# Optimization experiments

Hardware: AMD Instinct MI355X
Metric: run time of the kernel (lower is better)

## Reference

```python
import jax, jax.numpy as jnp
import numpy as np

EMBED_DIM = 1024
SCALE = 1.0 / float(np.sqrt(EMBED_DIM))


def setup_inputs() -> dict:
    key = jax.random.key(0)
    ks = jax.random.split(key, 7)
    B, S, D = 4, 2048, EMBED_DIM
    init = 1.0 / np.sqrt(D)
    x = jax.random.normal(ks[0], (B, S, D), dtype=jnp.float32)
    Wq = jax.random.uniform(ks[1], (D, D), jnp.float32, -init, init)
    bq = jax.random.uniform(ks[2], (D,), jnp.float32, -init, init)
    Wk = jax.random.uniform(ks[3], (D, D), jnp.float32, -init, init)
    bk = jax.random.uniform(ks[4], (D,), jnp.float32, -init, init)
    Wv = jax.random.uniform(ks[5], (D, D), jnp.float32, -init, init)
    bv = jax.random.uniform(ks[6], (D,), jnp.float32, -init, init)
    return {"x": x, "Wq": Wq, "bq": bq, "Wk": Wk, "bk": bk, "Wv": Wv, "bv": bv}


def reference(x, Wq, bq, Wk, bk, Wv, bv):
    # Linear projections (torch Linear: x @ W.T + b; here W stored as [in, out])
    q = x @ Wq + bq  # [B, S, D]
    k = x @ Wk + bk
    v = x @ Wv + bv
    # Manual scaled dot-product attention (single head)
    scores = jnp.einsum("bsd,btd->bst", q, k) * SCALE  # [B, S, S]
    attn = jax.nn.softmax(scores, axis=-1)
    # Dropout is identity at inference (eval mode); p=0.1 at train time.
    return jnp.einsum("bst,btd->bsd", attn, v)
```

## Files before the change

### kernel.cpp

```cpp
#include <hip/hip_runtime.h>

#define MODE_QKV 0
#define MODE_S   1
#define MODE_PV  2

typedef __attribute__((ext_vector_type(8))) short short8;
typedef __attribute__((ext_vector_type(4))) float floatx4;

typedef const unsigned __attribute__((address_space(1)))* gp_t;
typedef unsigned __attribute__((address_space(3)))* lp_t;

__device__ __forceinline__ void async16(const void* g, void* l) {
  __builtin_amdgcn_global_load_lds((gp_t)g, (lp_t)l, 16, 0, 0);
}

__device__ __forceinline__ unsigned short f2bf(float f) {
  union { float f; unsigned u; } x; x.f = f;
  unsigned r = x.u + 0x7fffu + ((x.u >> 16) & 1u);
  return (unsigned short)(r >> 16);
}
__device__ __forceinline__ float bf2f(unsigned short h) {
  union { unsigned u; float f; } x; x.u = ((unsigned)h) << 16;
  return x.f;
}


__device__ __forceinline__ void stage_half(const unsigned short* gp, long rowbase,
                                           int ldk, int kb, char* region,
                                           int wave, int lane) {
  const int rs = lane >> 3;
  const int kc = ((lane & 7) ^ rs) << 3;
  #pragma unroll
  for (int h = 0; h < 2; h++) {
    const int rr = (h * 8 + wave) * 8 + rs;
    async16(gp + (rowbase + rr) * (long)ldk + kb + kc,
            region + (h * 8 + wave) * 1024);
  }
}

__device__ __forceinline__ short8 frag(const char* region, int hr, int ks, int quad) {
  return *(const short8*)(region + hr * 128 + ((((ks << 2) | quad) ^ (hr & 7)) << 4));
}

#define MFMA_QUAD(MH, NH)                                                    \
  do {                                                                       \
    _Pragma("unroll")                                                        \
    for (int mi_ = 0; mi_ < 4; mi_++) {                                      \
      _Pragma("unroll")                                                      \
      for (int jj_ = 0; jj_ < 2; jj_++) {                                    \
        _Pragma("unroll")                                                    \
        for (int ks_ = 0; ks_ < 2; ks_++) {                                  \
          acc[MH][mi_][NH][jj_] = __builtin_amdgcn_mfma_f32_16x16x32_bf16(   \
              a[mi_][ks_], b[NH][jj_][ks_], acc[MH][mi_][NH][jj_], 0, 0, 0); \
        }                                                                    \
      }                                                                      \
    }                                                                        \
  } while (0)

template<int MODE>
__global__ __launch_bounds__(512, 1)
void gemm256(const unsigned short* __restrict__ A,
             const unsigned short* __restrict__ Bmat,
             const float* __restrict__ b0, const float* __restrict__ b1,
             const float* __restrict__ b2,
             unsigned short* __restrict__ O0, unsigned short* __restrict__ O1,
             unsigned short* __restrict__ O2, float* __restrict__ lsum,
             int M, int N, int K, long aZ, long bZ, long cZ, float scale)
{
  __shared__ __attribute__((aligned(128))) char lds[131072];

  const int tid = threadIdx.x;
  const int wave = tid >> 6, lane = tid & 63;
  const int wm = wave >> 2, wn = wave & 3;
  const int quad = lane >> 4, l16 = lane & 15;

  const int gx = gridDim.x, gy = gridDim.y;
  int z, bm, bn;
  {
    int f = (blockIdx.z * gy + blockIdx.y) * gx + blockIdx.x;
    int T = gx * gy * (int)gridDim.z;
    int nsq = T >> 7;
    int xcd = f & 7, i = f >> 3;
    int sq = xcd * nsq + (i >> 4);
    int w = i & 15;
    int spz = (gx >> 2) * (gy >> 2);
    z = sq / spz;
    int sqr = sq - z * spz;
    int sqm = sqr / (gx >> 2), sqn = sqr - sqm * (gx >> 2);
    bm = (sqm * 4 + (w >> 2)) * 256;
    bn = (sqn * 4 + (w & 3)) * 256;
  }

  const unsigned short* Ap = (MODE == MODE_QKV) ? A : (A + (long)z * aZ);
  const unsigned short* Bp = Bmat + (long)z * bZ;

  const int NT = K >> 6;

  stage_half(Ap, bm,       K, 0,  lds +     0, wave, lane);
  stage_half(Bp, bn,       K, 0,  lds + 32768, wave, lane);
  stage_half(Bp, bn + 128, K, 0,  lds + 49152, wave, lane);
  stage_half(Ap, bm + 128, K, 0,  lds + 16384, wave, lane);
  stage_half(Ap, bm,       K, 64, lds + 65536 +     0, wave, lane);
  stage_half(Bp, bn,       K, 64, lds + 65536 + 32768, wave, lane);
  stage_half(Bp, bn + 128, K, 64, lds + 65536 + 49152, wave, lane);
  asm volatile("s_waitcnt vmcnt(6)" ::: "memory");
  __builtin_amdgcn_s_barrier();

  floatx4 acc[2][4][2][2];
  #pragma unroll
  for (int p = 0; p < 2; p++)
    #pragma unroll
    for (int q2 = 0; q2 < 4; q2++)
      #pragma unroll
      for (int r = 0; r < 2; r++)
        #pragma unroll
        for (int s = 0; s < 2; s++)
          acc[p][q2][r][s] = (floatx4){0.f, 0.f, 0.f, 0.f};

  short8 a[4][2];
  short8 b[2][2][2];

  for (int j = 0; j < NT; j++) {
    char* bufc = lds + ((j & 1) << 16);
    char* bufn = lds + (((j + 1) & 1) << 16);
    const bool lp = (j + 2 >= NT);
    const int kn  = (j + 1) << 6;
    const int kn2 = (j + 2) << 6;

    #pragma unroll
    for (int mi = 0; mi < 4; mi++)
      #pragma unroll
      for (int ks = 0; ks < 2; ks++)
        a[mi][ks] = frag(bufc, wm * 64 + mi * 16 + l16, ks, quad);
    #pragma unroll
    for (int jj = 0; jj < 2; jj++)
      #pragma unroll
      for (int ks = 0; ks < 2; ks++)
        b[0][jj][ks] = frag(bufc + 32768, wn * 32 + jj * 16 + l16, ks, quad);
    if (j + 1 < NT)
      stage_half(Ap, bm + 128, K, kn, bufn + 16384, wave, lane);
    __builtin_amdgcn_s_barrier();
    asm volatile("s_waitcnt lgkmcnt(0)" ::: "memory");
    __builtin_amdgcn_sched_barrier(0);
    __builtin_amdgcn_s_setprio(1);
    MFMA_QUAD(0, 0);
    __builtin_amdgcn_s_setprio(0);
    __builtin_amdgcn_s_barrier();

    #pragma unroll
    for (int jj = 0; jj < 2; jj++)
      #pragma unroll
      for (int ks = 0; ks < 2; ks++)
        b[1][jj][ks] = frag(bufc + 49152, wn * 32 + jj * 16 + l16, ks, quad);
    if (!lp)
      stage_half(Ap, bm, K, kn2, bufc, wave, lane);
    __builtin_amdgcn_s_barrier();
    asm volatile("s_waitcnt lgkmcnt(0)" ::: "memory");
    __builtin_amdgcn_sched_barrier(0);
    __builtin_amdgcn_s_setprio(1);
    MFMA_QUAD(0, 1);
    __builtin_amdgcn_s_setprio(0);
    __builtin_amdgcn_s_barrier();

    #pragma unroll
    for (int mi = 0; mi < 4; mi++)
      #pragma unroll
      for (int ks = 0; ks < 2; ks++)
        a[mi][ks] = frag(bufc + 16384, wm * 64 + mi * 16 + l16, ks, quad);
    if (!lp)
      stage_half(Bp, bn, K, kn2, bufc + 32768, wave, lane);
    __builtin_amdgcn_s_barrier();
    asm volatile("s_waitcnt lgkmcnt(0)" ::: "memory");
    __builtin_amdgcn_sched_barrier(0);
    __builtin_amdgcn_s_setprio(1);
    MFMA_QUAD(1, 0);
    __builtin_amdgcn_s_setprio(0);
    __builtin_amdgcn_s_barrier();

    if (!lp) {
      stage_half(Bp, bn + 128, K, kn2, bufc + 49152, wave, lane);
      asm volatile("s_waitcnt vmcnt(6)" ::: "memory");
    } else {
      asm volatile("s_waitcnt vmcnt(0)" ::: "memory");
    }
    __builtin_amdgcn_s_barrier();
    __builtin_amdgcn_s_setprio(1);
    MFMA_QUAD(1, 1);
    __builtin_amdgcn_s_setprio(0);
    __builtin_amdgcn_s_barrier();
  }

  const bool vtrans = (MODE == MODE_QKV) && (z == 2);
  float bi[2][2];
  if (MODE == MODE_QKV) {
    const float* bias = (z == 0) ? b0 : ((z == 1) ? b1 : b2);
    #pragma unroll
    for (int nh = 0; nh < 2; nh++)
      #pragma unroll
      for (int jj = 0; jj < 2; jj++)
        bi[nh][jj] = bias[bn + nh * 128 + wn * 32 + jj * 16 + l16];
  }

  unsigned short* epi = (unsigned short*)lds;
  #pragma unroll
  for (int mh = 0; mh < 2; mh++) {
    #pragma unroll
    for (int mi = 0; mi < 4; mi++) {
      const int r0 = wm * 64 + mi * 16 + quad * 4;
      #pragma unroll
      for (int nh = 0; nh < 2; nh++)
        #pragma unroll
        for (int jj = 0; jj < 2; jj++) {
          const int col = nh * 128 + wn * 32 + jj * 16 + l16;
          if (MODE == MODE_S) {
            #pragma unroll
            for (int r = 0; r < 4; r++)
              epi[(r0 + r) * 264 + col] = f2bf(__expf(acc[mh][mi][nh][jj][r] * scale));
          } else if (!vtrans) {
            #pragma unroll
            for (int r = 0; r < 4; r++)
              epi[(r0 + r) * 264 + col] = f2bf(acc[mh][mi][nh][jj][r] + bi[nh][jj]);
          } else {
            #pragma unroll
            for (int r = 0; r < 4; r += 2) {
              unsigned lo = f2bf(acc[mh][mi][nh][jj][r] + bi[nh][jj]);
              unsigned hi = f2bf(acc[mh][mi][nh][jj][r + 1] + bi[nh][jj]);
              *(unsigned*)&epi[col * 136 + r0 + r] = lo | (hi << 16);
            }
          }
        }
    }
    __syncthreads();

    if (!vtrans) {
      #pragma unroll
      for (int it = 0; it < 8; it++) {
        int flat = it * 4096 + tid * 8;
        int rr = flat >> 8, cc = flat & 255;
        short8 vline = *(const short8*)&epi[rr * 264 + cc];
        long grow = bm + mh * 128 + rr;
        if (MODE == MODE_S) {
          union { short8 v; unsigned short u[8]; } t; t.v = vline;
          float s8 = 0.f;
          #pragma unroll
          for (int jq = 0; jq < 8; jq++) s8 += bf2f(t.u[jq]);
          s8 += __shfl_xor(s8, 1);
          s8 += __shfl_xor(s8, 2);
          s8 += __shfl_xor(s8, 4);
          s8 += __shfl_xor(s8, 8);
          s8 += __shfl_xor(s8, 16);
          if ((lane & 31) == 0) atomicAdd(&lsum[(long)z * M + grow], s8);
          *(short8*)&O0[(long)z * cZ + grow * N + bn + cc] = vline;
        } else {
          unsigned short* O = (z == 0) ? O0 : O1;
          *(short8*)&O[grow * N + bn + cc] = vline;
        }
      }
    } else {
      int bb = bm >> 11, s0 = bm & 2047;
      #pragma unroll
      for (int it = 0; it < 8; it++) {
        int flat = it * 4096 + tid * 8;
        int dd = flat >> 7, ss = flat & 127;
        short8 vline = *(const short8*)&epi[dd * 136 + ss];
        *(short8*)&O2[(long)bb * (1024L * 2048) + (long)(bn + dd) * 2048 + s0 + mh * 128 + ss] = vline;
      }
    }
    if (mh == 0) __syncthreads();
  }
}


union SmemU {
  struct { unsigned short A[2][4096]; unsigned short B[2][4096]; } st;
  unsigned short epi[128 * 136];
};

template<int MODE>
__global__ __launch_bounds__(256, 4)
void gemm_nt(const unsigned short* __restrict__ A,
             const unsigned short* __restrict__ Bmat,
             const float* __restrict__ b0, const float* __restrict__ b1,
             const float* __restrict__ b2,
             unsigned short* __restrict__ O0, unsigned short* __restrict__ O1,
             unsigned short* __restrict__ O2,
             float* __restrict__ Of, float* __restrict__ lsum,
             int M, int N, int K, long aZ, long bZ, long cZ, float scale)
{
  __shared__ SmemU smem;

  const int tid = threadIdx.x;
  const int wave = tid >> 6, lane = tid & 63;
  const int wm = wave >> 1, wn = wave & 1;
  const int quad = lane >> 4, l16 = lane & 15;

  const int gx = gridDim.x, gy = gridDim.y;
  int z, bm, bn;
  {
    int f = (blockIdx.z * gy + blockIdx.y) * gx + blockIdx.x;
    int T = gx * gy * (int)gridDim.z;
    int nsq = T >> 7;
    int xcd = f & 7, i = f >> 3;
    int sq = xcd * nsq + (i >> 4);
    int w = i & 15;
    int spz = (gx >> 2) * (gy >> 2);
    z = sq / spz;
    int sqr = sq - z * spz;
    int sqm = sqr / (gx >> 2), sqn = sqr - sqm * (gx >> 2);
    bm = (sqm * 4 + (w >> 2)) * 128;
    bn = (sqn * 4 + (w & 3)) * 128;
  }

  const unsigned short* Ap = (MODE == MODE_QKV) ? A : (A + (long)z * aZ);
  const unsigned short* Bp = Bmat + (long)z * bZ;

  floatx4 acc[4][4];
  #pragma unroll
  for (int i = 0; i < 4; i++)
    #pragma unroll
    for (int j = 0; j < 4; j++)
      acc[i][j] = (floatx4){0.f, 0.f, 0.f, 0.f};

  char* asb = (char*)&smem.st.A[0][0] + wave * 1024;
  char* bsb = (char*)&smem.st.B[0][0] + wave * 1024;

  for (int k0 = 0; k0 < K; k0 += 64) {
    #pragma unroll
    for (int p = 0; p < 2; p++) {
      #pragma unroll
      for (int h = 0; h < 2; h++) {
        int flat = tid + h * 256;
        int r = flat >> 2, c = (flat & 3) << 3;
        async16(Ap + (long)(bm + r) * K + k0 + p * 32 + c,
                asb + p * 8192 + h * 4096);
        async16(Bp + (long)(bn + r) * K + k0 + p * 32 + c,
                bsb + p * 8192 + h * 4096);
      }
    }
    __syncthreads();

    #pragma unroll
    for (int ks = 0; ks < 2; ks++) {
      short8 afr[4], bfr[4];
      #pragma unroll
      for (int i = 0; i < 4; i++)
        afr[i] = *(const short8*)&smem.st.A[ks][(wm * 64 + i * 16 + l16) * 32 + quad * 8];
      #pragma unroll
      for (int i = 0; i < 4; i++)
        bfr[i] = *(const short8*)&smem.st.B[ks][(wn * 64 + i * 16 + l16) * 32 + quad * 8];
      #pragma unroll
      for (int mi = 0; mi < 4; mi++)
        #pragma unroll
        for (int ni = 0; ni < 4; ni++)
          acc[mi][ni] = __builtin_amdgcn_mfma_f32_16x16x32_bf16(
              afr[mi], bfr[ni], acc[mi][ni], 0, 0, 0);
    }
    __syncthreads();
  }

  if (MODE == MODE_PV) {
    #pragma unroll
    for (int mi = 0; mi < 4; mi++) {
      int row0 = bm + wm * 64 + mi * 16 + quad * 4;
      float inv[4];
      #pragma unroll
      for (int r = 0; r < 4; r++)
        inv[r] = 1.0f / lsum[(long)z * M + row0 + r];
      #pragma unroll
      for (int ni = 0; ni < 4; ni++) {
        int col = bn + wn * 64 + ni * 16 + l16;
        #pragma unroll
        for (int r = 0; r < 4; r++)
          Of[(long)z * cZ + (long)(row0 + r) * N + col] = acc[mi][ni][r] * inv[r];
      }
    }
    return;
  }

  const bool vtrans = (MODE == MODE_QKV) && (z == 2);
  float bi[4];
  if (MODE == MODE_QKV) {
    const float* bias = (z == 0) ? b0 : ((z == 1) ? b1 : b2);
    #pragma unroll
    for (int ni = 0; ni < 4; ni++) bi[ni] = bias[bn + wn * 64 + ni * 16 + l16];
  }

  #pragma unroll
  for (int ni = 0; ni < 4; ni++) {
    int col = wn * 64 + ni * 16 + l16;
    float bb = (MODE == MODE_QKV) ? bi[ni] : 0.f;
    #pragma unroll
    for (int mi = 0; mi < 4; mi++) {
      int row0 = wm * 64 + mi * 16 + quad * 4;
      if (MODE == MODE_S) {
        #pragma unroll
        for (int r = 0; r < 4; r++)
          smem.epi[(row0 + r) * 136 + col] = f2bf(__expf(acc[mi][ni][r] * scale));
      } else if (!vtrans) {
        #pragma unroll
        for (int r = 0; r < 4; r++)
          smem.epi[(row0 + r) * 136 + col] = f2bf(acc[mi][ni][r] + bb);
      } else {
        #pragma unroll
        for (int r = 0; r < 4; r += 2) {
          unsigned lo = f2bf(acc[mi][ni][r] + bb);
          unsigned hi = f2bf(acc[mi][ni][r + 1] + bb);
          *(unsigned*)&smem.epi[col * 136 + row0 + r] = lo | (hi << 16);
        }
      }
    }
  }
  __syncthreads();

  #pragma unroll
  for (int i = 0; i < 8; i++) {
    int flat = i * 2048 + tid * 8;
    int rr = flat >> 7, cc = flat & 127;
    short8 vline = *(const short8*)&smem.epi[rr * 136 + cc];
    if (MODE == MODE_S) {
      union { short8 v; unsigned short u[8]; } t; t.v = vline;
      float s8 = 0.f;
      #pragma unroll
      for (int j = 0; j < 8; j++) s8 += bf2f(t.u[j]);
      s8 += __shfl_xor(s8, 1);
      s8 += __shfl_xor(s8, 2);
      s8 += __shfl_xor(s8, 4);
      s8 += __shfl_xor(s8, 8);
      if ((lane & 15) == 0) atomicAdd(&lsum[(long)z * M + bm + rr], s8);
      *(short8*)&O0[(long)z * cZ + (long)(bm + rr) * N + bn + cc] = vline;
    } else if (!vtrans) {
      unsigned short* O = (z == 0) ? O0 : O1;
      *(short8*)&O[(long)(bm + rr) * N + bn + cc] = vline;
    } else {
      int bb = bm >> 11, s0 = bm & 2047;
      *(short8*)&O2[(long)bb * (1024L * 2048) + (long)(bn + rr) * 2048 + s0 + cc] = vline;
    }
  }
}

__global__ __launch_bounds__(256)
void prep_kernel(const float* __restrict__ x, unsigned short* __restrict__ xb,
                 const float* __restrict__ W0, const float* __restrict__ W1,
                 const float* __restrict__ W2, unsigned short* __restrict__ Wt,
                 float* __restrict__ lsum) {
  int blk = blockIdx.x;
  if (blk < 4096) {
    long i = ((long)blk * 256 + threadIdx.x) * 8;
    float4 a = *(const float4*)(x + i);
    float4 b = *(const float4*)(x + i + 4);
    union { int4 v; unsigned short u[8]; } t;
    t.u[0] = f2bf(a.x); t.u[1] = f2bf(a.y); t.u[2] = f2bf(a.z); t.u[3] = f2bf(a.w);
    t.u[4] = f2bf(b.x); t.u[5] = f2bf(b.y); t.u[6] = f2bf(b.z); t.u[7] = f2bf(b.w);
    *(int4*)(xb + i) = t.v;
  } else if (blk < 7168) {
    __shared__ float tile[32][33];
    int tt = blk - 4096;
    int zz = tt >> 10, rem = tt & 1023;
    int kb = (rem >> 5) * 32, nb = (rem & 31) * 32;
    const float* W = (zz == 0) ? W0 : ((zz == 1) ? W1 : W2);
    unsigned short* O = Wt + (long)zz * 1024 * 1024;
    int t = threadIdx.x, tr = t >> 5, tc = t & 31;
    #pragma unroll
    for (int i = 0; i < 4; i++)
      tile[tr + i * 8][tc] = W[(long)(kb + tr + i * 8) * 1024 + nb + tc];
    __syncthreads();
    #pragma unroll
    for (int i = 0; i < 4; i++)
      O[(long)(nb + tr + i * 8) * 1024 + kb + tc] = f2bf(tile[tc][tr + i * 8]);
  } else {
    int i = (blk - 7168) * 256 + threadIdx.x;
    lsum[i] = 0.f;
  }
}

extern "C" void kernel_launch(void* const* d_in, const int* in_sizes, int n_in,
                              void* d_out, int out_size, void* d_ws, size_t ws_size,
                              hipStream_t stream) {
  const float* x  = (const float*)d_in[0];
  const float* Wq = (const float*)d_in[1];
  const float* bq = (const float*)d_in[2];
  const float* Wk = (const float*)d_in[3];
  const float* bk = (const float*)d_in[4];
  const float* Wv = (const float*)d_in[5];
  const float* bv = (const float*)d_in[6];
  float* out = (float*)d_out;

  const int B = 4, S = 2048, D = 1024;
  const int M = B * S;
  const float scale = 0.03125f;

  unsigned short* xb = (unsigned short*)d_out;
  unsigned short* Wt = xb + (size_t)M * D;
  unsigned short* q  = (unsigned short*)d_ws;
  unsigned short* k  = q + (size_t)M * D;
  unsigned short* vT = k + (size_t)M * D;
  unsigned short* P  = vT + (size_t)M * D;

  size_t need_full = ((size_t)3 * M * D + (size_t)B * S * S) * sizeof(unsigned short)
                   + (size_t)M * sizeof(float);
  const bool full = (ws_size >= need_full);
  float* lsum = full ? (float*)(P + (size_t)B * S * S)
                     : (float*)(P + (size_t)S * S);

  prep_kernel<<<7200, 256, 0, stream>>>(x, xb, Wq, Wk, Wv, Wt, lsum);

  gemm256<MODE_QKV><<<dim3(D / 256, M / 256, 3), 512, 0, stream>>>(
      xb, Wt, bq, bk, bv, q, k, vT, nullptr,
      M, D, D, 0, (long)D * D, 0, 1.0f);

  if (full) {
    gemm256<MODE_S><<<dim3(S / 256, S / 256, B), 512, 0, stream>>>(
        q, k, nullptr, nullptr, nullptr, P, nullptr, nullptr, lsum,
        S, S, D, (long)S * D, (long)S * D, (long)S * S, scale);
    gemm_nt<MODE_PV><<<dim3(D / 128, S / 128, B), 256, 0, stream>>>(
        P, vT, nullptr, nullptr, nullptr, nullptr, nullptr, nullptr, out, lsum,
        S, D, S, (long)S * S, (long)D * S, (long)S * D, 1.0f);
  } else {
    for (int b = 0; b < B; b++) {
      const unsigned short* qb = q + (size_t)b * S * D;
      const unsigned short* kb = k + (size_t)b * S * D;
      const unsigned short* vb = vT + (size_t)b * S * D;
      float* ob = out + (size_t)b * S * D;
      gemm_nt<MODE_S><<<dim3(S / 128, S / 128, 1), 256, 0, stream>>>(
          qb, kb, nullptr, nullptr, nullptr, P, nullptr, nullptr, nullptr,
          lsum + (size_t)b * S,
          S, S, D, 0, 0, 0, scale);
      gemm_nt<MODE_PV><<<dim3(D / 128, S / 128, 1), 256, 0, stream>>>(
          P, vb, nullptr, nullptr, nullptr, nullptr, nullptr, nullptr, ob,
          lsum + (size_t)b * S,
          S, D, S, 0, 0, 0, 1.0f);
    }
  }
}
```

Baseline: 242.5 us.

## Run PV GEMM with 256x256 tiled kernel and drop sched barriers

The PV product (P times V^T) now uses the 256x256-tile, 512-thread pipelined gemm256 kernel instead of the 128x128 gemm_nt kernel. A new MODE_PV epilogue normalizes each row by the softmax row sum and writes fp32 output directly. Separately, the sched_barrier calls inside the main loop are removed so the compiler can interleave LDS fragment loads with MFMAs. The larger tiles improve operand reuse, but the grid shrinks to 4x8x4 = 128 blocks, which may underfill the GPU, and the epilogue writes are strided fp32 stores.

```diff
diff --git a/kernel.cpp b/kernel.cpp
--- a/kernel.cpp
+++ b/kernel.cpp
@@ -64,7 +64,8 @@
              const float* __restrict__ b0, const float* __restrict__ b1,
              const float* __restrict__ b2,
              unsigned short* __restrict__ O0, unsigned short* __restrict__ O1,
-             unsigned short* __restrict__ O2, float* __restrict__ lsum,
+             unsigned short* __restrict__ O2, float* __restrict__ Of,
+             float* __restrict__ lsum,
              int M, int N, int K, long aZ, long bZ, long cZ, float scale)
 {
   __shared__ __attribute__((aligned(128))) char lds[131072];
@@ -141,7 +142,6 @@
       stage_half(Ap, bm + 128, K, kn, bufn + 16384, wave, lane);
     __builtin_amdgcn_s_barrier();
     asm volatile("s_waitcnt lgkmcnt(0)" ::: "memory");
-    __builtin_amdgcn_sched_barrier(0);
     __builtin_amdgcn_s_setprio(1);
     MFMA_QUAD(0, 0);
     __builtin_amdgcn_s_setprio(0);
@@ -156,7 +156,6 @@
       stage_half(Ap, bm, K, kn2, bufc, wave, lane);
     __builtin_amdgcn_s_barrier();
     asm volatile("s_waitcnt lgkmcnt(0)" ::: "memory");
-    __builtin_amdgcn_sched_barrier(0);
     __builtin_amdgcn_s_setprio(1);
     MFMA_QUAD(0, 1);
     __builtin_amdgcn_s_setprio(0);
@@ -171,7 +170,6 @@
       stage_half(Bp, bn, K, kn2, bufc + 32768, wave, lane);
     __builtin_amdgcn_s_barrier();
     asm volatile("s_waitcnt lgkmcnt(0)" ::: "memory");
-    __builtin_amdgcn_sched_barrier(0);
     __builtin_amdgcn_s_setprio(1);
     MFMA_QUAD(1, 0);
     __builtin_amdgcn_s_setprio(0);
@@ -188,6 +186,30 @@
     MFMA_QUAD(1, 1);
     __builtin_amdgcn_s_setprio(0);
     __builtin_amdgcn_s_barrier();
+  }
+
+  if (MODE == MODE_PV) {
+    #pragma unroll
+    for (int mh = 0; mh < 2; mh++)
+      #pragma unroll
+      for (int mi = 0; mi < 4; mi++) {
+        const int row0 = bm + mh * 128 + wm * 64 + mi * 16 + quad * 4;
+        float inv[4];
+        #pragma unroll
+        for (int r = 0; r < 4; r++)
+          inv[r] = 1.0f / lsum[(long)z * M + row0 + r];
+        #pragma unroll
+        for (int nh = 0; nh < 2; nh++)
+          #pragma unroll
+          for (int jj = 0; jj < 2; jj++) {
+            const int col = bn + nh * 128 + wn * 32 + jj * 16 + l16;
+            #pragma unroll
+            for (int r = 0; r < 4; r++)
+              Of[(long)z * cZ + (long)(row0 + r) * N + col] =
+                  acc[mh][mi][nh][jj][r] * inv[r];
+          }
+      }
+    return;
   }
 
   const bool vtrans = (MODE == MODE_QKV) && (z == 2);
@@ -505,14 +527,14 @@
   prep_kernel<<<7200, 256, 0, stream>>>(x, xb, Wq, Wk, Wv, Wt, lsum);
 
   gemm256<MODE_QKV><<<dim3(D / 256, M / 256, 3), 512, 0, stream>>>(
-      xb, Wt, bq, bk, bv, q, k, vT, nullptr,
+      xb, Wt, bq, bk, bv, q, k, vT, nullptr, nullptr,
       M, D, D, 0, (long)D * D, 0, 1.0f);
 
   if (full) {
     gemm256<MODE_S><<<dim3(S / 256, S / 256, B), 512, 0, stream>>>(
-        q, k, nullptr, nullptr, nullptr, P, nullptr, nullptr, lsum,
+        q, k, nullptr, nullptr, nullptr, P, nullptr, nullptr, nullptr, lsum,
         S, S, D, (long)S * D, (long)S * D, (long)S * S, scale);
-    gemm_nt<MODE_PV><<<dim3(D / 128, S / 128, B), 256, 0, stream>>>(
+    gemm256<MODE_PV><<<dim3(D / 256, S / 256, B), 512, 0, stream>>>(
         P, vT, nullptr, nullptr, nullptr, nullptr, nullptr, nullptr, out, lsum,
         S, D, S, (long)S * S, (long)D * S, (long)S * D, 1.0f);
   } else {
```

Result: slower. 258.3 us (+6.5%).
